# Kernel optimization log

Measured on AMD Instinct MI355X. Metric: run time of the kernel, lower is better.

## Reference

```python
import jax, jax.numpy as jnp
import numpy as np

SIG = [1, 1, 1, 1, -1]  # Cl(4,1)
GA_DIM = 1 << len(SIG)  # 32
IN_F, OUT_F = 128, 128
EPS = 1e-6


def _cayley(sig):
    """Dense Cayley tensor C[a,b,k]: e_a * e_b = C[a,b,a^b] * e_{a^b}.
    Only dim^2 of the dim^3 entries are nonzero (one k per (a,b))."""
    n = len(sig)
    dim = 1 << n
    C = np.zeros((dim, dim, dim), dtype=np.float32)
    for a in range(dim):
        for b in range(dim):
            # reordering sign from moving b's generators past a's
            s = 0
            aa = a >> 1
            while aa:
                s += bin(aa & b).count('1')
                aa >>= 1
            sign = -1.0 if (s & 1) else 1.0
            # metric contribution from repeated generators
            common = a & b
            for i in range(n):
                if common & (1 << i):
                    sign *= sig[i]
            C[a, b, a ^ b] = sign
    return C

_C = jnp.asarray(_cayley(SIG))  # [32,32,32]


def setup_inputs() -> dict:
    key = jax.random.key(0)
    kx, kw = jax.random.split(key)
    x = jax.random.normal(kx, (4096, IN_F, GA_DIM), dtype=jnp.float32)
    std = (2.0 / (IN_F * GA_DIM)) ** 0.5
    w = jax.random.normal(kw, (OUT_F, IN_F, GA_DIM), dtype=jnp.float32) * std
    return {"x": x, "weight": w}


def reference(x, weight):
    # Fold Cayley table into the weight once: Wc[o,f,i,k] = sum_j W[o,f,j] C[i,j,k]
    Wc = jnp.einsum('ofj,ijk->ofik', weight, _C)
    # Geometric linear layer: y[b,o,k] = sum_{f,i} x[b,f,i] Wc[o,f,i,k]
    y = jnp.einsum('bfi,ofik->bok', x, Wc)
    # Manifold normalization: project each output multivector to unit norm
    inv = jax.lax.rsqrt(jnp.sum(y * y, axis=-1, keepdims=True) + EPS)
    return y * inv
```

## Files before the change

kernel.cpp:

```cpp
#include <hip/hip_runtime.h>
#include <stdint.h>

typedef unsigned short ushort_t;
typedef __attribute__((ext_vector_type(8))) __bf16 bf16x8;
typedef __attribute__((ext_vector_type(4))) float  f32x4;


__device__ __forceinline__ unsigned int f2bf(float f) {
    unsigned int u = __float_as_uint(f);
    return (u + 0x7FFFu + ((u >> 16) & 1u)) >> 16;
}

__device__ __forceinline__ float cayley_sign(int a, int b) {
    int s = 0;
    int aa = a >> 1;
    while (aa) { s += __popc(aa & b); aa >>= 1; }
    float sign = (s & 1) ? -1.0f : 1.0f;
    if (a & b & 16) sign = -sign;
    return sign;
}

__device__ __forceinline__ void async16(const ushort_t* g, const ushort_t* l) {
    const __attribute__((address_space(1))) unsigned int* gp =
        (const __attribute__((address_space(1))) unsigned int*)(uintptr_t)g;
    __attribute__((address_space(3))) unsigned int* lp =
        (__attribute__((address_space(3))) unsigned int*)(unsigned int)(uintptr_t)l;
    __builtin_amdgcn_global_load_lds(gp, lp, 16, 0, 0);
}

__global__ __launch_bounds__(256) void prepAB(const float* __restrict__ x,
                                              const float* __restrict__ w,
                                              ushort_t* __restrict__ A_sw,
                                              ushort_t* __restrict__ B_sw) {
    const int k_blk = blockIdx.x;
    const int p_blk = blockIdx.y >> 1;
    const int sub   = blockIdx.y & 1;
    const int t = threadIdx.x;
    const int r  = sub * 64 + (t >> 2);
    const int kq = t & 3;

    const int kt = k_blk >> 1;
    const int kh = k_blk & 1;

    if (blockIdx.z == 0) {
        const int R = p_blk * 128 + r;
        const float* src = x + (size_t)R * 4096 + (size_t)k_blk * 32 + kq * 8;
        float4 a = ((const float4*)src)[0];
        float4 b = ((const float4*)src)[1];
        uint4 pk;
        pk.x = f2bf(a.x) | (f2bf(a.y) << 16);
        pk.y = f2bf(a.z) | (f2bf(a.w) << 16);
        pk.z = f2bf(b.x) | (f2bf(b.y) << 16);
        pk.w = f2bf(b.z) | (f2bf(b.w) << 16);
        const int P = R >> 8, rowp = R & 255;
        *(uint4*)(A_sw + (size_t)(P * 64 + kt) * 16384 + kh * 8192 + kq * 2048 + rowp * 8) = pk;
    } else {
        const int n = p_blk * 128 + r;
        const int o = n >> 5;
        const int kc = n & 31;
        const float* wrow = w + (size_t)o * 4096 + (size_t)k_blk * 32;
        unsigned int pk[4];
#pragma unroll
        for (int pr = 0; pr < 4; ++pr) {
            const int i0 = kq * 8 + pr * 2, i1 = i0 + 1;
            const int j0 = i0 ^ kc, j1 = i1 ^ kc;
            float v0 = wrow[j0] * cayley_sign(i0, j0);
            float v1 = wrow[j1] * cayley_sign(i1, j1);
            pk[pr] = f2bf(v0) | (f2bf(v1) << 16);
        }
        uint4 u = {pk[0], pk[1], pk[2], pk[3]};
        const int P = n >> 8, colp = n & 255;
        *(uint4*)(B_sw + (size_t)(P * 64 + kt) * 16384 + kh * 8192 + kq * 2048 + colp * 8) = u;
    }
}


#define MFMA16(a, b, c) __builtin_amdgcn_mfma_f32_16x16x32_bf16(a, b, c, 0, 0, 0)

#define RD_A4(d0, d1, d2, d3, base, KH, TMB) do {                              \
        const ushort_t* _p = (base) + aOff + (KH) * 8192 + (TMB) * 128;        \
        d0 = *(const bf16x8*)(_p + 0 * 128);                                   \
        d1 = *(const bf16x8*)(_p + 1 * 128);                                   \
        d2 = *(const bf16x8*)(_p + 2 * 128);                                   \
        d3 = *(const bf16x8*)(_p + 3 * 128);                                   \
    } while (0)

#define RD_B4(d0, d1, d2, d3, base, KH) do {                                   \
        const ushort_t* _p = (base) + bOff + (KH) * 8192;                      \
        d0 = *(const bf16x8*)(_p + 0 * 128);                                   \
        d1 = *(const bf16x8*)(_p + 1 * 128);                                   \
        d2 = *(const bf16x8*)(_p + 2 * 128);                                   \
        d3 = *(const bf16x8*)(_p + 3 * 128);                                   \
    } while (0)

#define PHASE(STAGE_STMT, RD_STMT, TMB, A0, A1, A2, A3, TAIL)                  \
    {                                                                          \
        STAGE_STMT;                                                            \
        RD_STMT;                                                               \
        __builtin_amdgcn_sched_barrier(0);                                     \
        __builtin_amdgcn_s_setprio(1);                                         \
        acc[(TMB) + 0][0] = MFMA16(A0, B0_, acc[(TMB) + 0][0]);                \
        acc[(TMB) + 0][1] = MFMA16(A0, B1_, acc[(TMB) + 0][1]);                \
        acc[(TMB) + 0][2] = MFMA16(A0, B2_, acc[(TMB) + 0][2]);                \
        acc[(TMB) + 0][3] = MFMA16(A0, B3_, acc[(TMB) + 0][3]);                \
        acc[(TMB) + 1][0] = MFMA16(A1, B0_, acc[(TMB) + 1][0]);                \
        acc[(TMB) + 1][1] = MFMA16(A1, B1_, acc[(TMB) + 1][1]);                \
        acc[(TMB) + 1][2] = MFMA16(A1, B2_, acc[(TMB) + 1][2]);                \
        acc[(TMB) + 1][3] = MFMA16(A1, B3_, acc[(TMB) + 1][3]);                \
        acc[(TMB) + 2][0] = MFMA16(A2, B0_, acc[(TMB) + 2][0]);                \
        acc[(TMB) + 2][1] = MFMA16(A2, B1_, acc[(TMB) + 2][1]);                \
        acc[(TMB) + 2][2] = MFMA16(A2, B2_, acc[(TMB) + 2][2]);                \
        acc[(TMB) + 2][3] = MFMA16(A2, B3_, acc[(TMB) + 2][3]);                \
        acc[(TMB) + 3][0] = MFMA16(A3, B0_, acc[(TMB) + 3][0]);                \
        acc[(TMB) + 3][1] = MFMA16(A3, B1_, acc[(TMB) + 3][1]);                \
        acc[(TMB) + 3][2] = MFMA16(A3, B2_, acc[(TMB) + 3][2]);                \
        acc[(TMB) + 3][3] = MFMA16(A3, B3_, acc[(TMB) + 3][3]);                \
        __builtin_amdgcn_s_setprio(0);                                         \
        TAIL;                                                                  \
        __builtin_amdgcn_s_barrier();                                          \
    }

__global__ __launch_bounds__(512, 2) void gemm_norm(const ushort_t* __restrict__ A_sw,
                                                    const ushort_t* __restrict__ B_sw,
                                                    float* __restrict__ out) {
    __shared__ ushort_t As[2][16384];
    __shared__ ushort_t Bs[2][16384];

    int id = blockIdx.x;
    id = (id & 7) * 32 + (id >> 3);
    const int m_blk = id >> 4;
    const int n_blk = id & 15;

    const int t    = threadIdx.x;
    const int wave = t >> 6;
    const int lane = t & 63;
    const int wr = wave >> 2;
    const int wc = wave & 3;
    const int lg = lane >> 4;
    const int lm = lane & 15;

    const int aOff = (lg * 256 + wr * 128 + lm) * 8;
    const int bOff = (lg * 256 + wc * 64  + lm) * 8;

    const ushort_t* aPanel = A_sw + (size_t)m_blk * 64 * 16384;
    const ushort_t* bPanel = B_sw + (size_t)n_blk * 64 * 16384;

    f32x4 acc[8][4];
#pragma unroll
    for (int i = 0; i < 8; ++i)
#pragma unroll
        for (int j = 0; j < 4; ++j)
#pragma unroll
            for (int k = 0; k < 4; ++k) acc[i][j][k] = 0.0f;

    const int so = wave * 1024 + lane * 8;
    const int sl = wave * 1024;

    auto STAGE2 = [&](const ushort_t* src, ushort_t* ldsb) {
        async16(src + so,       ldsb + sl);
        async16(src + so + 512, ldsb + sl + 512);
    };

    const int NT = 64;

    STAGE2(bPanel + 0,             &Bs[0][0]);
    STAGE2(aPanel + 0,             &As[0][0]);
    STAGE2(bPanel + 8192,          &Bs[0][8192]);
    STAGE2(aPanel + 8192,          &As[0][8192]);
    STAGE2(bPanel + 16384,         &Bs[1][0]);
    STAGE2(aPanel + 16384,         &As[1][0]);
    STAGE2(bPanel + 16384 + 8192,  &Bs[1][8192]);
    asm volatile("s_waitcnt vmcnt(10)" ::: "memory");
    __builtin_amdgcn_s_barrier();

    bf16x8 aX0, aX1, aX2, aX3, aY0, aY1, aY2, aY3;
    bf16x8 bX0, bX1, bX2, bX3, bY0, bY1, bY2, bY3;

    RD_A4(aX0, aX1, aX2, aX3, &As[0][0], 0, 0);
    RD_B4(bX0, bX1, bX2, bX3, &Bs[0][0], 0);

#define B0_ bX0
#define B1_ bX1
#define B2_ bX2
#define B3_ bX3
#define C0_ bY0
#define C1_ bY1
#define C2_ bY2
#define C3_ bY3

#pragma unroll 2
    for (int tt = 0; tt < NT - 2; ++tt) {
        const int b = tt & 1;
        const ushort_t* Ac = &As[b][0];
        const ushort_t* Bc = &Bs[b][0];
        const ushort_t* An = &As[b ^ 1][0];
        const ushort_t* Bn = &Bs[b ^ 1][0];

        PHASE(STAGE2(aPanel + (size_t)(tt + 1) * 16384 + 8192, &As[b ^ 1][8192]),
              RD_A4(aY0, aY1, aY2, aY3, Ac, 0, 4),
              0, aX0, aX1, aX2, aX3,
              asm volatile("s_waitcnt vmcnt(8)" ::: "memory"))

        PHASE(STAGE2(bPanel + (size_t)(tt + 2) * 16384, &Bs[b][0]),
              RD_A4(aX0, aX1, aX2, aX3, Ac, 1, 0); RD_B4(bY0, bY1, bY2, bY3, Bc, 1),
              4, aY0, aY1, aY2, aY3,
              {})

#undef B0_
#undef B1_
#undef B2_
#undef B3_
#define B0_ bY0
#define B1_ bY1
#define B2_ bY2
#define B3_ bY3

        PHASE(STAGE2(aPanel + (size_t)(tt + 2) * 16384, &As[b][0]),
              RD_A4(aY0, aY1, aY2, aY3, Ac, 1, 4),
              0, aX0, aX1, aX2, aX3,
              asm volatile("s_waitcnt vmcnt(8)" ::: "memory"))

        PHASE(STAGE2(bPanel + (size_t)(tt + 2) * 16384 + 8192, &Bs[b][8192]),
              RD_A4(aX0, aX1, aX2, aX3, An, 0, 0); RD_B4(bX0, bX1, bX2, bX3, Bn, 0),
              4, aY0, aY1, aY2, aY3,
              {})

#undef B0_
#undef B1_
#undef B2_
#undef B3_
#define B0_ bX0
#define B1_ bX1
#define B2_ bX2
#define B3_ bX3
    }

    {
        const ushort_t* Ac = &As[0][0];
        const ushort_t* Bc = &Bs[0][0];
        const ushort_t* An = &As[1][0];
        const ushort_t* Bn = &Bs[1][0];

        PHASE(STAGE2(aPanel + (size_t)(NT - 1) * 16384 + 8192, &As[1][8192]),
              RD_A4(aY0, aY1, aY2, aY3, Ac, 0, 4),
              0, aX0, aX1, aX2, aX3,
              asm volatile("s_waitcnt vmcnt(8)" ::: "memory"))
        PHASE({},
              RD_A4(aX0, aX1, aX2, aX3, Ac, 1, 0); RD_B4(bY0, bY1, bY2, bY3, Bc, 1),
              4, aY0, aY1, aY2, aY3,
              {})
#undef B0_
#undef B1_
#undef B2_
#undef B3_
#define B0_ bY0
#define B1_ bY1
#define B2_ bY2
#define B3_ bY3
        PHASE({},
              RD_A4(aY0, aY1, aY2, aY3, Ac, 1, 4),
              0, aX0, aX1, aX2, aX3,
              asm volatile("s_waitcnt vmcnt(4)" ::: "memory"))
        PHASE({},
              RD_A4(aX0, aX1, aX2, aX3, An, 0, 0); RD_B4(bX0, bX1, bX2, bX3, Bn, 0),
              4, aY0, aY1, aY2, aY3,
              {})
#undef B0_
#undef B1_
#undef B2_
#undef B3_
#define B0_ bX0
#define B1_ bX1
#define B2_ bX2
#define B3_ bX3
    }
    {
        const ushort_t* Ac = &As[1][0];
        const ushort_t* Bc = &Bs[1][0];

        PHASE({},
              RD_A4(aY0, aY1, aY2, aY3, Ac, 0, 4),
              0, aX0, aX1, aX2, aX3,
              asm volatile("s_waitcnt vmcnt(0)" ::: "memory"))
        PHASE({},
              RD_A4(aX0, aX1, aX2, aX3, Ac, 1, 0); RD_B4(bY0, bY1, bY2, bY3, Bc, 1),
              4, aY0, aY1, aY2, aY3,
              {})
#undef B0_
#undef B1_
#undef B2_
#undef B3_
#define B0_ bY0
#define B1_ bY1
#define B2_ bY2
#define B3_ bY3
        PHASE({},
              RD_A4(aY0, aY1, aY2, aY3, Ac, 1, 4),
              0, aX0, aX1, aX2, aX3,
              {})
        {
            __builtin_amdgcn_s_setprio(1);
            acc[4][0] = MFMA16(aY0, B0_, acc[4][0]);
            acc[4][1] = MFMA16(aY0, B1_, acc[4][1]);
            acc[4][2] = MFMA16(aY0, B2_, acc[4][2]);
            acc[4][3] = MFMA16(aY0, B3_, acc[4][3]);
            acc[5][0] = MFMA16(aY1, B0_, acc[5][0]);
            acc[5][1] = MFMA16(aY1, B1_, acc[5][1]);
            acc[5][2] = MFMA16(aY1, B2_, acc[5][2]);
            acc[5][3] = MFMA16(aY1, B3_, acc[5][3]);
            acc[6][0] = MFMA16(aY2, B0_, acc[6][0]);
            acc[6][1] = MFMA16(aY2, B1_, acc[6][1]);
            acc[6][2] = MFMA16(aY2, B2_, acc[6][2]);
            acc[6][3] = MFMA16(aY2, B3_, acc[6][3]);
            acc[7][0] = MFMA16(aY3, B0_, acc[7][0]);
            acc[7][1] = MFMA16(aY3, B1_, acc[7][1]);
            acc[7][2] = MFMA16(aY3, B2_, acc[7][2]);
            acc[7][3] = MFMA16(aY3, B3_, acc[7][3]);
            __builtin_amdgcn_s_setprio(0);
        }
    }

    const int row0 = m_blk * 256 + wr * 128;
    const int col0 = n_blk * 256 + wc * 64;
#pragma unroll
    for (int tm = 0; tm < 8; ++tm) {
#pragma unroll
        for (int u = 0; u < 2; ++u) {
#pragma unroll
            for (int reg = 0; reg < 4; ++reg) {
                float v0 = acc[tm][2 * u][reg];
                float v1 = acc[tm][2 * u + 1][reg];
                float p = v0 * v0 + v1 * v1;
                p += __shfl_xor(p, 1);
                p += __shfl_xor(p, 2);
                p += __shfl_xor(p, 4);
                p += __shfl_xor(p, 8);
                const float inv = rsqrtf(p + 1e-6f);
                const int row = row0 + tm * 16 + lg * 4 + reg;
                float* orow = out + (size_t)row * 4096 + col0 + u * 32 + lm;
                orow[0]  = v0 * inv;
                orow[16] = v1 * inv;
            }
        }
    }
}


extern "C" void kernel_launch(void* const* d_in, const int* in_sizes, int n_in,
                              void* d_out, int out_size, void* d_ws, size_t ws_size,
                              hipStream_t stream) {
    const float* x = (const float*)d_in[0];
    const float* w = (const float*)d_in[1];
    float* out = (float*)d_out;

    ushort_t* A_sw = (ushort_t*)d_ws;
    ushort_t* B_sw = A_sw + (size_t)4096 * 4096;

    prepAB<<<dim3(128, 64, 2), 256, 0, stream>>>(x, w, A_sw, B_sw);
    gemm_norm<<<dim3(256), 512, 0, stream>>>(A_sw, B_sw, out);
}
```

Before: 229.4 us.

## Fuse x-to-bf16 conversion into GEMM, loading fp32 A directly into registers

Removes the separate pass that converted x to a swizzled bf16 workspace. The GEMM now loads fp32 x tiles straight from global memory into registers, converts them to bf16 and writes them into LDS inside the pipelined main loop. B still uses async global-to-LDS loads. This saves a full write and re-read of a 32MB intermediate, but it doubles A-side global traffic per tile, since fp32 is fetched and each x tile is reread by all 16 n-blocks. It also adds register pressure and VALU conversion work inside the loop.

```diff
diff --git a/kernel.cpp b/kernel.cpp
--- a/kernel.cpp
+++ b/kernel.cpp
@@ -9,6 +9,9 @@
 __device__ __forceinline__ unsigned int f2bf(float f) {
     unsigned int u = __float_as_uint(f);
     return (u + 0x7FFFu + ((u >> 16) & 1u)) >> 16;
+}
+__device__ __forceinline__ unsigned int pk2bf(float lo, float hi) {
+    return f2bf(lo) | (f2bf(hi) << 16);
 }
 
 __device__ __forceinline__ float cayley_sign(int a, int b) {
@@ -28,10 +31,8 @@
     __builtin_amdgcn_global_load_lds(gp, lp, 16, 0, 0);
 }
 
-__global__ __launch_bounds__(256) void prepAB(const float* __restrict__ x,
-                                              const float* __restrict__ w,
-                                              ushort_t* __restrict__ A_sw,
-                                              ushort_t* __restrict__ B_sw) {
+__global__ __launch_bounds__(256) void prepB(const float* __restrict__ w,
+                                             ushort_t* __restrict__ B_sw) {
     const int k_blk = blockIdx.x;
     const int p_blk = blockIdx.y >> 1;
     const int sub   = blockIdx.y & 1;
@@ -42,36 +43,22 @@
     const int kt = k_blk >> 1;
     const int kh = k_blk & 1;
 
-    if (blockIdx.z == 0) {
-        const int R = p_blk * 128 + r;
-        const float* src = x + (size_t)R * 4096 + (size_t)k_blk * 32 + kq * 8;
-        float4 a = ((const float4*)src)[0];
-        float4 b = ((const float4*)src)[1];
-        uint4 pk;
-        pk.x = f2bf(a.x) | (f2bf(a.y) << 16);
-        pk.y = f2bf(a.z) | (f2bf(a.w) << 16);
-        pk.z = f2bf(b.x) | (f2bf(b.y) << 16);
-        pk.w = f2bf(b.z) | (f2bf(b.w) << 16);
-        const int P = R >> 8, rowp = R & 255;
-        *(uint4*)(A_sw + (size_t)(P * 64 + kt) * 16384 + kh * 8192 + kq * 2048 + rowp * 8) = pk;
-    } else {
-        const int n = p_blk * 128 + r;
-        const int o = n >> 5;
-        const int kc = n & 31;
-        const float* wrow = w + (size_t)o * 4096 + (size_t)k_blk * 32;
-        unsigned int pk[4];
-#pragma unroll
-        for (int pr = 0; pr < 4; ++pr) {
-            const int i0 = kq * 8 + pr * 2, i1 = i0 + 1;
-            const int j0 = i0 ^ kc, j1 = i1 ^ kc;
-            float v0 = wrow[j0] * cayley_sign(i0, j0);
-            float v1 = wrow[j1] * cayley_sign(i1, j1);
-            pk[pr] = f2bf(v0) | (f2bf(v1) << 16);
-        }
-        uint4 u = {pk[0], pk[1], pk[2], pk[3]};
-        const int P = n >> 8, colp = n & 255;
-        *(uint4*)(B_sw + (size_t)(P * 64 + kt) * 16384 + kh * 8192 + kq * 2048 + colp * 8) = u;
-    }
+    const int n = p_blk * 128 + r;
+    const int o = n >> 5;
+    const int kc = n & 31;
+    const float* wrow = w + (size_t)o * 4096 + (size_t)k_blk * 32;
+    unsigned int pk[4];
+#pragma unroll
+    for (int pr = 0; pr < 4; ++pr) {
+        const int i0 = kq * 8 + pr * 2, i1 = i0 + 1;
+        const int j0 = i0 ^ kc, j1 = i1 ^ kc;
+        float v0 = wrow[j0] * cayley_sign(i0, j0);
+        float v1 = wrow[j1] * cayley_sign(i1, j1);
+        pk[pr] = f2bf(v0) | (f2bf(v1) << 16);
+    }
+    uint4 u = {pk[0], pk[1], pk[2], pk[3]};
+    const int P = n >> 8, colp = n & 255;
+    *(uint4*)(B_sw + (size_t)(P * 64 + kt) * 16384 + kh * 8192 + kq * 2048 + colp * 8) = u;
 }
 
 
@@ -91,6 +78,22 @@
         d1 = *(const bf16x8*)(_p + 1 * 128);                                   \
         d2 = *(const bf16x8*)(_p + 2 * 128);                                   \
         d3 = *(const bf16x8*)(_p + 3 * 128);                                   \
+    } while (0)
+
+#define A_ISSUE(S0, S1, S2, S3, T, H) do {                                     \
+        const float* _s = xbase + (size_t)(T) * 64 + (H) * 32;                 \
+        S0 = *(const float4*)_s;           S1 = *(const float4*)(_s + 4);      \
+        S2 = *(const float4*)(_s + 65536); S3 = *(const float4*)(_s + 65536 + 4); \
+    } while (0)
+
+#define A_WRITE(S0, S1, S2, S3, BUF, H) do {                                   \
+        uint4 _p0, _p1;                                                        \
+        _p0.x = pk2bf(S0.x, S0.y); _p0.y = pk2bf(S0.z, S0.w);                  \
+        _p0.z = pk2bf(S1.x, S1.y); _p0.w = pk2bf(S1.z, S1.w);                  \
+        _p1.x = pk2bf(S2.x, S2.y); _p1.y = pk2bf(S2.z, S2.w);                  \
+        _p1.z = pk2bf(S3.x, S3.y); _p1.w = pk2bf(S3.z, S3.w);                  \
+        ushort_t* _d = &As[BUF][(H) * 8192 + awOff];                           \
+        *(uint4*)_d = _p0; *(uint4*)(_d + 128) = _p1;                          \
     } while (0)
 
 #define PHASE(STAGE_STMT, RD_STMT, TMB, A0, A1, A2, A3, TAIL)                  \
@@ -120,7 +123,7 @@
         __builtin_amdgcn_s_barrier();                                          \
     }
 
-__global__ __launch_bounds__(512, 2) void gemm_norm(const ushort_t* __restrict__ A_sw,
+__global__ __launch_bounds__(512, 2) void gemm_norm(const float* __restrict__ x,
                                                     const ushort_t* __restrict__ B_sw,
                                                     float* __restrict__ out) {
     __shared__ ushort_t As[2][16384];
@@ -141,8 +144,10 @@
 
     const int aOff = (lg * 256 + wr * 128 + lm) * 8;
     const int bOff = (lg * 256 + wc * 64  + lm) * 8;
-
-    const ushort_t* aPanel = A_sw + (size_t)m_blk * 64 * 16384;
+    const int awOff = (lane & 3) * 2048 + (wave * 32 + (lane >> 2)) * 8;
+
+    const float* xbase = x + (size_t)(m_blk * 256 + wave * 32 + (lane >> 2)) * 4096
+                           + (lane & 3) * 8;
     const ushort_t* bPanel = B_sw + (size_t)n_blk * 64 * 16384;
 
     f32x4 acc[8][4];
@@ -155,22 +160,26 @@
 
     const int so = wave * 1024 + lane * 8;
     const int sl = wave * 1024;
-
-    auto STAGE2 = [&](const ushort_t* src, ushort_t* ldsb) {
+    auto STAGE2B = [&](const ushort_t* src, ushort_t* ldsb) {
         async16(src + so,       ldsb + sl);
         async16(src + so + 512, ldsb + sl + 512);
     };
 
     const int NT = 64;
-
-    STAGE2(bPanel + 0,             &Bs[0][0]);
-    STAGE2(aPanel + 0,             &As[0][0]);
-    STAGE2(bPanel + 8192,          &Bs[0][8192]);
-    STAGE2(aPanel + 8192,          &As[0][8192]);
-    STAGE2(bPanel + 16384,         &Bs[1][0]);
-    STAGE2(aPanel + 16384,         &As[1][0]);
-    STAGE2(bPanel + 16384 + 8192,  &Bs[1][8192]);
-    asm volatile("s_waitcnt vmcnt(10)" ::: "memory");
+    float4 P0, P1, P2, P3, Q0, Q1, Q2, Q3;
+
+    STAGE2B(bPanel + 0,             &Bs[0][0]);
+    STAGE2B(bPanel + 8192,          &Bs[0][8192]);
+    STAGE2B(bPanel + 16384,         &Bs[1][0]);
+    STAGE2B(bPanel + 16384 + 8192,  &Bs[1][8192]);
+    A_ISSUE(Q0, Q1, Q2, Q3, 0, 0);
+    A_ISSUE(P0, P1, P2, P3, 0, 1);
+    A_WRITE(Q0, Q1, Q2, Q3, 0, 0);
+    A_WRITE(P0, P1, P2, P3, 0, 1);
+    A_ISSUE(Q0, Q1, Q2, Q3, 1, 0);
+    A_WRITE(Q0, Q1, Q2, Q3, 1, 0);
+    A_ISSUE(P0, P1, P2, P3, 1, 1);
+    asm volatile("s_waitcnt vmcnt(4) lgkmcnt(0)" ::: "memory");
     __builtin_amdgcn_s_barrier();
 
     bf16x8 aX0, aX1, aX2, aX3, aY0, aY1, aY2, aY3;
@@ -183,10 +192,6 @@
 #define B1_ bX1
 #define B2_ bX2
 #define B3_ bX3
-#define C0_ bY0
-#define C1_ bY1
-#define C2_ bY2
-#define C3_ bY3
 
 #pragma unroll 2
     for (int tt = 0; tt < NT - 2; ++tt) {
@@ -196,12 +201,12 @@
         const ushort_t* An = &As[b ^ 1][0];
         const ushort_t* Bn = &Bs[b ^ 1][0];
 
-        PHASE(STAGE2(aPanel + (size_t)(tt + 1) * 16384 + 8192, &As[b ^ 1][8192]),
+        PHASE({ A_WRITE(P0, P1, P2, P3, b ^ 1, 1); A_ISSUE(Q0, Q1, Q2, Q3, tt + 2, 0); },
               RD_A4(aY0, aY1, aY2, aY3, Ac, 0, 4),
               0, aX0, aX1, aX2, aX3,
-              asm volatile("s_waitcnt vmcnt(8)" ::: "memory"))
-
-        PHASE(STAGE2(bPanel + (size_t)(tt + 2) * 16384, &Bs[b][0]),
+              asm volatile("s_waitcnt lgkmcnt(0)" ::: "memory"))
+
+        PHASE(STAGE2B(bPanel + (size_t)(tt + 2) * 16384, &Bs[b][0]),
               RD_A4(aX0, aX1, aX2, aX3, Ac, 1, 0); RD_B4(bY0, bY1, bY2, bY3, Bc, 1),
               4, aY0, aY1, aY2, aY3,
               {})
@@ -215,12 +220,12 @@
 #define B2_ bY2
 #define B3_ bY3
 
-        PHASE(STAGE2(aPanel + (size_t)(tt + 2) * 16384, &As[b][0]),
+        PHASE({ A_WRITE(Q0, Q1, Q2, Q3, b, 0); A_ISSUE(P0, P1, P2, P3, tt + 2, 1); },
               RD_A4(aY0, aY1, aY2, aY3, Ac, 1, 4),
               0, aX0, aX1, aX2, aX3,
-              asm volatile("s_waitcnt vmcnt(8)" ::: "memory"))
-
-        PHASE(STAGE2(bPanel + (size_t)(tt + 2) * 16384 + 8192, &Bs[b][8192]),
+              asm volatile("s_waitcnt lgkmcnt(0)" ::: "memory"))
+
+        PHASE(STAGE2B(bPanel + (size_t)(tt + 2) * 16384 + 8192, &Bs[b][8192]),
               RD_A4(aX0, aX1, aX2, aX3, An, 0, 0); RD_B4(bX0, bX1, bX2, bX3, Bn, 0),
               4, aY0, aY1, aY2, aY3,
               {})
@@ -241,10 +246,10 @@
         const ushort_t* An = &As[1][0];
         const ushort_t* Bn = &Bs[1][0];
 
-        PHASE(STAGE2(aPanel + (size_t)(NT - 1) * 16384 + 8192, &As[1][8192]),
+        PHASE(A_WRITE(P0, P1, P2, P3, 1, 1),
               RD_A4(aY0, aY1, aY2, aY3, Ac, 0, 4),
               0, aX0, aX1, aX2, aX3,
-              asm volatile("s_waitcnt vmcnt(8)" ::: "memory"))
+              asm volatile("s_waitcnt lgkmcnt(0)" ::: "memory"))
         PHASE({},
               RD_A4(aX0, aX1, aX2, aX3, Ac, 1, 0); RD_B4(bY0, bY1, bY2, bY3, Bc, 1),
               4, aY0, aY1, aY2, aY3,
@@ -260,11 +265,11 @@
         PHASE({},
               RD_A4(aY0, aY1, aY2, aY3, Ac, 1, 4),
               0, aX0, aX1, aX2, aX3,
-              asm volatile("s_waitcnt vmcnt(4)" ::: "memory"))
+              {})
         PHASE({},
               RD_A4(aX0, aX1, aX2, aX3, An, 0, 0); RD_B4(bX0, bX1, bX2, bX3, Bn, 0),
               4, aY0, aY1, aY2, aY3,
-              {})
+              asm volatile("s_waitcnt vmcnt(0)" ::: "memory"))
 #undef B0_
 #undef B1_
 #undef B2_
@@ -281,7 +286,7 @@
         PHASE({},
               RD_A4(aY0, aY1, aY2, aY3, Ac, 0, 4),
               0, aX0, aX1, aX2, aX3,
-              asm volatile("s_waitcnt vmcnt(0)" ::: "memory"))
+              {})
         PHASE({},
               RD_A4(aX0, aX1, aX2, aX3, Ac, 1, 0); RD_B4(bY0, bY1, bY2, bY3, Bc, 1),
               4, aY0, aY1, aY2, aY3,
@@ -353,9 +358,8 @@
     const float* w = (const float*)d_in[1];
     float* out = (float*)d_out;
 
-    ushort_t* A_sw = (ushort_t*)d_ws;
-    ushort_t* B_sw = A_sw + (size_t)4096 * 4096;
-
-    prepAB<<<dim3(128, 64, 2), 256, 0, stream>>>(x, w, A_sw, B_sw);
-    gemm_norm<<<dim3(256), 512, 0, stream>>>(A_sw, B_sw, out);
-}
+    ushort_t* B_sw = (ushort_t*)d_ws;
+
+    prepB<<<dim3(128, 64), 256, 0, stream>>>(w, B_sw);
+    gemm_norm<<<dim3(256), 512, 0, stream>>>(x, B_sw, out);
+}
```

Result: slower. 292.0 us (+27.3%).

## Fuse bf16 prep pass into GEMM kernel via cooperative grid sync

Applied to the files above, without the earlier changes.

Merges the separate conversion/Cayley-folding prep kernel into the GEMM+normalization kernel, launched cooperatively with a grid-wide sync between the prep phase and the GEMM phase. The intent is to remove one kernel launch and the inter-kernel gap. In exchange, the prep phase now runs with only 256 blocks of 512 threads in grid-stride loops, and the grid sync adds a barrier cost. The prep work may also have less parallelism than it had as a standalone kernel.

```diff
diff --git a/kernel.cpp b/kernel.cpp
--- a/kernel.cpp
+++ b/kernel.cpp
@@ -1,5 +1,8 @@
 #include <hip/hip_runtime.h>
+#include <hip/hip_cooperative_groups.h>
 #include <stdint.h>
+
+namespace cg = cooperative_groups;
 
 typedef unsigned short ushort_t;
 typedef __attribute__((ext_vector_type(8))) __bf16 bf16x8;
@@ -26,52 +29,6 @@
     __attribute__((address_space(3))) unsigned int* lp =
         (__attribute__((address_space(3))) unsigned int*)(unsigned int)(uintptr_t)l;
     __builtin_amdgcn_global_load_lds(gp, lp, 16, 0, 0);
-}
-
-__global__ __launch_bounds__(256) void prepAB(const float* __restrict__ x,
-                                              const float* __restrict__ w,
-                                              ushort_t* __restrict__ A_sw,
-                                              ushort_t* __restrict__ B_sw) {
-    const int k_blk = blockIdx.x;
-    const int p_blk = blockIdx.y >> 1;
-    const int sub   = blockIdx.y & 1;
-    const int t = threadIdx.x;
-    const int r  = sub * 64 + (t >> 2);
-    const int kq = t & 3;
-
-    const int kt = k_blk >> 1;
-    const int kh = k_blk & 1;
-
-    if (blockIdx.z == 0) {
-        const int R = p_blk * 128 + r;
-        const float* src = x + (size_t)R * 4096 + (size_t)k_blk * 32 + kq * 8;
-        float4 a = ((const float4*)src)[0];
-        float4 b = ((const float4*)src)[1];
-        uint4 pk;
-        pk.x = f2bf(a.x) | (f2bf(a.y) << 16);
-        pk.y = f2bf(a.z) | (f2bf(a.w) << 16);
-        pk.z = f2bf(b.x) | (f2bf(b.y) << 16);
-        pk.w = f2bf(b.z) | (f2bf(b.w) << 16);
-        const int P = R >> 8, rowp = R & 255;
-        *(uint4*)(A_sw + (size_t)(P * 64 + kt) * 16384 + kh * 8192 + kq * 2048 + rowp * 8) = pk;
-    } else {
-        const int n = p_blk * 128 + r;
-        const int o = n >> 5;
-        const int kc = n & 31;
-        const float* wrow = w + (size_t)o * 4096 + (size_t)k_blk * 32;
-        unsigned int pk[4];
-#pragma unroll
-        for (int pr = 0; pr < 4; ++pr) {
-            const int i0 = kq * 8 + pr * 2, i1 = i0 + 1;
-            const int j0 = i0 ^ kc, j1 = i1 ^ kc;
-            float v0 = wrow[j0] * cayley_sign(i0, j0);
-            float v1 = wrow[j1] * cayley_sign(i1, j1);
-            pk[pr] = f2bf(v0) | (f2bf(v1) << 16);
-        }
-        uint4 u = {pk[0], pk[1], pk[2], pk[3]};
-        const int P = n >> 8, colp = n & 255;
-        *(uint4*)(B_sw + (size_t)(P * 64 + kt) * 16384 + kh * 8192 + kq * 2048 + colp * 8) = u;
-    }
 }
 
 
@@ -120,11 +77,75 @@
         __builtin_amdgcn_s_barrier();                                          \
     }
 
-__global__ __launch_bounds__(512, 2) void gemm_norm(const ushort_t* __restrict__ A_sw,
-                                                    const ushort_t* __restrict__ B_sw,
-                                                    float* __restrict__ out) {
+
+__global__ __launch_bounds__(512, 2) void fused_versor(const float* __restrict__ x,
+                                                       const float* __restrict__ w,
+                                                       ushort_t* __restrict__ A_sw,
+                                                       ushort_t* __restrict__ B_sw,
+                                                       float* __restrict__ out) {
     __shared__ ushort_t As[2][16384];
     __shared__ ushort_t Bs[2][16384];
+
+    {
+        const int rtid = blockIdx.x * 512 + threadIdx.x;
+#pragma unroll 1
+        for (int it = 0; it < 16; ++it) {
+            const int v  = rtid + it * 131072;
+            const int tu = v & 255;
+            const int vb = v >> 8;
+            const int k_blk = vb & 127;
+            const int y  = vb >> 7;
+            const int p_blk = y >> 1, sub = y & 1;
+            const int r  = sub * 64 + (tu >> 2);
+            const int kq = tu & 3;
+            const int kt = k_blk >> 1, kh = k_blk & 1;
+
+            const int R = p_blk * 128 + r;
+            const float* src = x + (size_t)R * 4096 + (size_t)k_blk * 32 + kq * 8;
+            float4 a = ((const float4*)src)[0];
+            float4 b = ((const float4*)src)[1];
+            uint4 pk;
+            pk.x = f2bf(a.x) | (f2bf(a.y) << 16);
+            pk.y = f2bf(a.z) | (f2bf(a.w) << 16);
+            pk.z = f2bf(b.x) | (f2bf(b.y) << 16);
+            pk.w = f2bf(b.z) | (f2bf(b.w) << 16);
+            const int P = R >> 8, rowp = R & 255;
+            *(uint4*)(A_sw + (size_t)(P * 64 + kt) * 16384 + kh * 8192 + kq * 2048 + rowp * 8) = pk;
+        }
+#pragma unroll 1
+        for (int it = 0; it < 16; ++it) {
+            const int v  = rtid + it * 131072;
+            const int tu = v & 255;
+            const int vb = v >> 8;
+            const int k_blk = vb & 127;
+            const int y  = vb >> 7;
+            const int p_blk = y >> 1, sub = y & 1;
+            const int r  = sub * 64 + (tu >> 2);
+            const int kq = tu & 3;
+            const int kt = k_blk >> 1, kh = k_blk & 1;
+
+            const int n = p_blk * 128 + r;
+            const int o = n >> 5;
+            const int kc = n & 31;
+            const float* wrow = w + (size_t)o * 4096 + (size_t)k_blk * 32;
+            unsigned int pk[4];
+#pragma unroll
+            for (int pr = 0; pr < 4; ++pr) {
+                const int i0 = kq * 8 + pr * 2, i1 = i0 + 1;
+                const int j0 = i0 ^ kc, j1 = i1 ^ kc;
+                float v0 = wrow[j0] * cayley_sign(i0, j0);
+                float v1 = wrow[j1] * cayley_sign(i1, j1);
+                pk[pr] = f2bf(v0) | (f2bf(v1) << 16);
+            }
+            uint4 u = {pk[0], pk[1], pk[2], pk[3]};
+            const int P = n >> 8, colp = n & 255;
+            *(uint4*)(B_sw + (size_t)(P * 64 + kt) * 16384 + kh * 8192 + kq * 2048 + colp * 8) = u;
+        }
+    }
+
+    __threadfence();
+    cg::this_grid().sync();
+    __threadfence();
 
     int id = blockIdx.x;
     id = (id & 7) * 32 + (id >> 3);
@@ -183,10 +204,6 @@
 #define B1_ bX1
 #define B2_ bX2
 #define B3_ bX3
-#define C0_ bY0
-#define C1_ bY1
-#define C2_ bY2
-#define C3_ bY3
 
 #pragma unroll 2
     for (int tt = 0; tt < NT - 2; ++tt) {
@@ -356,6 +373,12 @@
     ushort_t* A_sw = (ushort_t*)d_ws;
     ushort_t* B_sw = A_sw + (size_t)4096 * 4096;
 
-    prepAB<<<dim3(128, 64, 2), 256, 0, stream>>>(x, w, A_sw, B_sw);
-    gemm_norm<<<dim3(256), 512, 0, stream>>>(A_sw, B_sw, out);
-}
+    void* args[5];
+    args[0] = (void*)&x;
+    args[1] = (void*)&w;
+    args[2] = (void*)&A_sw;
+    args[3] = (void*)&B_sw;
+    args[4] = (void*)&out;
+    hipLaunchCooperativeKernel((const void*)fused_versor, dim3(256), dim3(512),
+                               args, 0, stream);
+}
```

New measurement: 355.5 us. 55.0% more time.

## Halve per-phase barriers by batching A/B stages and waiting every two phases

Applied to the files above, without the earlier changes.

The main loop drops the barrier after every MFMA phase and issues the A and B half-panel async loads together. It now waits on vmcnt and synchronises only every second phase. The prologue also stages one fewer chunk before entering the loop. This is meant to cut barrier and waitcnt stalls between waves, at the risk of reading LDS before loads land or overwriting buffers still being read if the reduced synchronisation is insufficient.

```diff
diff --git a/kernel.cpp b/kernel.cpp
--- a/kernel.cpp
+++ b/kernel.cpp
@@ -117,8 +117,12 @@
         acc[(TMB) + 3][3] = MFMA16(A3, B3_, acc[(TMB) + 3][3]);                \
         __builtin_amdgcn_s_setprio(0);                                         \
         TAIL;                                                                  \
-        __builtin_amdgcn_s_barrier();                                          \
-    }
+    }
+
+#define TAIL_BAR4  { asm volatile("s_waitcnt vmcnt(4)" ::: "memory");          \
+                     __builtin_amdgcn_s_barrier(); }
+#define TAIL_BAR0  { asm volatile("s_waitcnt vmcnt(0)" ::: "memory");          \
+                     __builtin_amdgcn_s_barrier(); }
 
 __global__ __launch_bounds__(512, 2) void gemm_norm(const ushort_t* __restrict__ A_sw,
                                                     const ushort_t* __restrict__ B_sw,
@@ -163,14 +167,13 @@
 
     const int NT = 64;
 
-    STAGE2(bPanel + 0,             &Bs[0][0]);
-    STAGE2(aPanel + 0,             &As[0][0]);
-    STAGE2(bPanel + 8192,          &Bs[0][8192]);
-    STAGE2(aPanel + 8192,          &As[0][8192]);
-    STAGE2(bPanel + 16384,         &Bs[1][0]);
-    STAGE2(aPanel + 16384,         &As[1][0]);
-    STAGE2(bPanel + 16384 + 8192,  &Bs[1][8192]);
-    asm volatile("s_waitcnt vmcnt(10)" ::: "memory");
+    STAGE2(aPanel + 0,      &As[0][0]);
+    STAGE2(bPanel + 0,      &Bs[0][0]);
+    STAGE2(aPanel + 8192,   &As[0][8192]);
+    STAGE2(bPanel + 8192,   &Bs[0][8192]);
+    STAGE2(aPanel + 16384,  &As[1][0]);
+    STAGE2(bPanel + 16384,  &Bs[1][0]);
+    asm volatile("s_waitcnt vmcnt(4)" ::: "memory");
     __builtin_amdgcn_s_barrier();
 
     bf16x8 aX0, aX1, aX2, aX3, aY0, aY1, aY2, aY3;
@@ -183,10 +186,6 @@
 #define B1_ bX1
 #define B2_ bX2
 #define B3_ bX3
-#define C0_ bY0
-#define C1_ bY1
-#define C2_ bY2
-#define C3_ bY3
 
 #pragma unroll 2
     for (int tt = 0; tt < NT - 2; ++tt) {
@@ -196,15 +195,16 @@
         const ushort_t* An = &As[b ^ 1][0];
         const ushort_t* Bn = &Bs[b ^ 1][0];
 
-        PHASE(STAGE2(aPanel + (size_t)(tt + 1) * 16384 + 8192, &As[b ^ 1][8192]),
+        PHASE({ STAGE2(aPanel + (size_t)(tt + 1) * 16384 + 8192, &As[b ^ 1][8192]);
+                STAGE2(bPanel + (size_t)(tt + 1) * 16384 + 8192, &Bs[b ^ 1][8192]); },
               RD_A4(aY0, aY1, aY2, aY3, Ac, 0, 4),
               0, aX0, aX1, aX2, aX3,
-              asm volatile("s_waitcnt vmcnt(8)" ::: "memory"))
-
-        PHASE(STAGE2(bPanel + (size_t)(tt + 2) * 16384, &Bs[b][0]),
+              {})
+
+        PHASE({},
               RD_A4(aX0, aX1, aX2, aX3, Ac, 1, 0); RD_B4(bY0, bY1, bY2, bY3, Bc, 1),
               4, aY0, aY1, aY2, aY3,
-              {})
+              TAIL_BAR4)
 
 #undef B0_
 #undef B1_
@@ -215,15 +215,16 @@
 #define B2_ bY2
 #define B3_ bY3
 
-        PHASE(STAGE2(aPanel + (size_t)(tt + 2) * 16384, &As[b][0]),
+        PHASE({ STAGE2(aPanel + (size_t)(tt + 2) * 16384, &As[b][0]);
+                STAGE2(bPanel + (size_t)(tt + 2) * 16384, &Bs[b][0]); },
               RD_A4(aY0, aY1, aY2, aY3, Ac, 1, 4),
               0, aX0, aX1, aX2, aX3,
-              asm volatile("s_waitcnt vmcnt(8)" ::: "memory"))
-
-        PHASE(STAGE2(bPanel + (size_t)(tt + 2) * 16384 + 8192, &Bs[b][8192]),
+              {})
+
+        PHASE({},
               RD_A4(aX0, aX1, aX2, aX3, An, 0, 0); RD_B4(bX0, bX1, bX2, bX3, Bn, 0),
               4, aY0, aY1, aY2, aY3,
-              {})
+              TAIL_BAR4)
 
 #undef B0_
 #undef B1_
@@ -241,14 +242,15 @@
         const ushort_t* An = &As[1][0];
         const ushort_t* Bn = &Bs[1][0];
 
-        PHASE(STAGE2(aPanel + (size_t)(NT - 1) * 16384 + 8192, &As[1][8192]),
+        PHASE({ STAGE2(aPanel + (size_t)(NT - 1) * 16384 + 8192, &As[1][8192]);
+                STAGE2(bPanel + (size_t)(NT - 1) * 16384 + 8192, &Bs[1][8192]); },
               RD_A4(aY0, aY1, aY2, aY3, Ac, 0, 4),
               0, aX0, aX1, aX2, aX3,
-              asm volatile("s_waitcnt vmcnt(8)" ::: "memory"))
+              {})
         PHASE({},
               RD_A4(aX0, aX1, aX2, aX3, Ac, 1, 0); RD_B4(bY0, bY1, bY2, bY3, Bc, 1),
               4, aY0, aY1, aY2, aY3,
-              {})
+              TAIL_BAR4)
 #undef B0_
 #undef B1_
 #undef B2_
@@ -260,11 +262,11 @@
         PHASE({},
               RD_A4(aY0, aY1, aY2, aY3, Ac, 1, 4),
               0, aX0, aX1, aX2, aX3,
-              asm volatile("s_waitcnt vmcnt(4)" ::: "memory"))
+              {})
         PHASE({},
               RD_A4(aX0, aX1, aX2, aX3, An, 0, 0); RD_B4(bX0, bX1, bX2, bX3, Bn, 0),
               4, aY0, aY1, aY2, aY3,
-              {})
+              TAIL_BAR0)
 #undef B0_
 #undef B1_
 #undef B2_
@@ -281,7 +283,7 @@
         PHASE({},
               RD_A4(aY0, aY1, aY2, aY3, Ac, 0, 4),
               0, aX0, aX1, aX2, aX3,
-              asm volatile("s_waitcnt vmcnt(0)" ::: "memory"))
+              {})
         PHASE({},
               RD_A4(aX0, aX1, aX2, aX3, Ac, 1, 0); RD_B4(bY0, bY1, bY2, bY3, Bc, 1),
               4, aY0, aY1, aY2, aY3,
```

After: 231.8 us. No clear change (+1.1%).
